# Optimization experiments

Measured on AMD Instinct MI355X. Metric: run time of the kernel, lower is better.

## Reference

```python
import jax, jax.numpy as jnp
import numpy as np

GELU = lambda v: jax.nn.gelu(v, approximate=False)  # torch nn.GELU default (exact erf)


def _gconv(x, w):
    # grouped conv1d, valid padding; w: (C,1,K), groups=C. lax conv = cross-correlation, same as torch.
    return jax.lax.conv_general_dilated(x, w, (1,), [(0, 0)],
                                        dimension_numbers=('NCH', 'OIH', 'NCH'),
                                        feature_group_count=x.shape[1])


def _conv(x, w, b):
    # dense conv1d, kernel 3, padding=1
    y = jax.lax.conv_general_dilated(x, w, (1,), [(1, 1)],
                                     dimension_numbers=('NCH', 'OIH', 'NCH'))
    return y + b[None, :, None]


def setup_inputs() -> dict:
    key = jax.random.key(0)
    ks = jax.random.split(key, 12)
    B, C, L = 8, 64, 2048
    H, FL, HD, TD, level = 32, 8, 64, 16, 3
    Cs = (1 + level) * C  # 256 channels into the ODE
    n = lambda k, s: (jax.random.normal(k, s) * 0.05).astype(jnp.float32)
    z = lambda s: jnp.zeros(s, jnp.float32)
    return dict(
        x=jax.random.normal(ks[0], (B, C, L), jnp.float32),
        # DyWAN_QR params
        sw1=n(ks[1], (H, C)), sb1=z((H,)),
        sw2=n(ks[2], (H, H)), sb2=z((H,)),
        sw3=n(ks[3], (2 * FL, H)), sb3=z((2 * FL,)),
        # ODE time embed / FiLM params
        tw1=n(ks[4], (TD, 1)), tb1=z((TD,)),
        tw2=n(ks[5], (TD, TD)), tb2=z((TD,)),
        cw=n(ks[6], (2 * HD, TD)), cb=z((2 * HD,)),
        # ODE conv stack params
        k1=n(ks[7], (HD, Cs, 3)), kb1=z((HD,)),
        k2=n(ks[8], (HD, HD, 3)), kb2=z((HD,)),
        k3=n(ks[9], (Cs, HD, 3)), kb3=z((Cs,)),
    )


def reference(x, sw1, sb1, sw2, sb2, sw3, sb3, tw1, tb1, tw2, tb2, cw, cb,
              k1, kb1, k2, kb2, k3, kb3):
    B, C, L = x.shape
    level, FL, T = 3, 8, 5

    def dywan(a):
        # stat_net: adaptive max pool over L -> (B,C) -> Linear -> GELU
        feat = GELU(jnp.max(a, axis=-1) @ sw1.T + sb1)
        raw = GELU(feat @ sw2.T + sb2) @ sw3.T + sb3  # (B, 2*FL)
        lo_raw, hi_raw = raw[:, :FL], raw[:, FL:]
        # QR of an (FL,1) column vector == L2 normalization (up to LAPACK sign)
        lo = lo_raw / jnp.linalg.norm(lo_raw, axis=1, keepdims=True)
        hi = hi_raw / jnp.linalg.norm(hi_raw, axis=1, keepdims=True)
        return lo, hi

    pad = FL - 1
    coeffs = [x]
    approx = x
    for _ in range(level):
        lo, hi = dywan(approx)
        lo_f = jnp.broadcast_to(lo.mean(0)[None, None, :], (C, 1, FL))
        hi_f = jnp.broadcast_to(hi.mean(0)[None, None, :], (C, 1, FL))
        ap = jnp.pad(approx, ((0, 0), (0, 0), (pad // 2, pad - pad // 2)), mode='reflect')
        new_approx = _gconv(ap, lo_f)[..., :L]
        coeffs.append(_gconv(ap, hi_f)[..., :L])
        approx = new_approx
    stacked = jnp.concatenate(coeffs, axis=1)  # (B, (1+level)*C, L)

    def ode_f(t, y):
        te = jnp.reshape(t, (1, 1)).astype(y.dtype)
        te = GELU(te @ tw1.T + tb1) @ tw2.T + tb2          # (1, TD)
        cond = te @ cw.T + cb                               # (1, 2*HD)
        hd = cond.shape[1] // 2
        gamma, beta = cond[:, :hd], cond[:, hd:]
        h = _conv(y, k1, kb1)
        h = (1.0 + gamma[:, :, None]) * h + beta[:, :, None]  # FiLM
        h = GELU(h)
        h = GELU(_conv(h, k2, kb2))
        return _conv(h, k3, kb3)

    # dopri5 tableau, fixed grid over linspace(0, 1, T) (b7 = 0, so 6 stages)
    hs = 1.0 / (T - 1)
    y = stacked
    for i in range(T - 1):
        t0 = i * hs
        s1 = ode_f(t0, y)
        s2 = ode_f(t0 + hs / 5, y + hs * (1 / 5) * s1)
        s3 = ode_f(t0 + 3 * hs / 10, y + hs * (3 / 40 * s1 + 9 / 40 * s2))
        s4 = ode_f(t0 + 4 * hs / 5, y + hs * (44 / 45 * s1 - 56 / 15 * s2 + 32 / 9 * s3))
        s5 = ode_f(t0 + 8 * hs / 9, y + hs * (19372 / 6561 * s1 - 25360 / 2187 * s2
                                              + 64448 / 6561 * s3 - 212 / 729 * s4))
        s6 = ode_f(t0 + hs, y + hs * (9017 / 3168 * s1 - 355 / 33 * s2 + 46732 / 5247 * s3
                                      + 49 / 176 * s4 - 5103 / 18656 * s5))
        y = y + hs * (35 / 384 * s1 + 500 / 1113 * s3 + 125 / 192 * s4
                      - 2187 / 6784 * s5 + 11 / 84 * s6)
    ode_out = y

    yl = ode_out[:, :C, :]
    yh0 = ode_out[:, C:2 * C, :]
    yh1 = ode_out[:, 2 * C:3 * C, :]
    yh2 = ode_out[:, 3 * C:4 * C, :]

    dx = ode_f(jnp.float32(1.0), ode_out)
    inner = jnp.sum(stacked * dx, axis=(1, 2))  # (B,)
    ecloss = jnp.mean(inner ** 2)
    return (yl, yh0, yh1, yh2, ecloss)
```

## Files before the change

kernel.cpp:

```cpp
#include <hip/hip_runtime.h>
#include <math.h>

#define B 8
#define C 64
#define L 2048
#define CS 256
#define BCL  (B*C*L)
#define BCSL (B*CS*L)
#define HS 0.25f

typedef unsigned short u16;
typedef unsigned int   u32;
typedef __attribute__((ext_vector_type(8))) short sh8;
typedef __attribute__((ext_vector_type(4))) float f4;
typedef __attribute__((ext_vector_type(8))) unsigned short us8;
typedef __attribute__((ext_vector_type(4))) unsigned short us4;

__device__ __forceinline__ float gelu(float x) {
    return 0.5f * x * (1.0f + erff(x * 0.70710678118654752440f));
}
__device__ __forceinline__ u16 f2b(float f) {
    u32 u = __float_as_uint(f);
    u32 r = u + 0x7FFFu + ((u >> 16) & 1u);
    return (u16)(r >> 16);
}
__device__ __forceinline__ float b2f(u16 h) {
    return __uint_as_float(((u32)h) << 16);
}
__device__ __forceinline__ u32 encmax(float f) {
    u32 b = __float_as_uint(f);
    return (b & 0x80000000u) ? ~b : (b | 0x80000000u);
}
__device__ __forceinline__ float decmax(u32 u) {
    return __uint_as_float((u & 0x80000000u) ? (u ^ 0x80000000u) : ~u);
}

struct ComboB { const u16* p[6]; float c[6]; };

__device__ __forceinline__ void ldw_a6(const sh8* __restrict__ w, int cb, int g,
                                       int lane, sh8 (&A)[6]) {
    #pragma unroll
    for (int u = 0; u < 6; ++u) A[u] = w[((cb + u)*4 + g)*64 + lane];
}

__global__ __launch_bounds__(256) void prep_k(const float* __restrict__ w,
        u16* __restrict__ dst, int IC, int OC) {
    int idx = blockIdx.x * 256 + threadIdx.x;
    int OCG = OC >> 4;
    int j = idx & 7, lane = (idx >> 3) & 63, t = idx >> 9;
    int ocg = t % OCG, c = t / OCG;
    int oc = ocg * 16 + (lane & 15);
    int K = c * 32 + ((lane >> 4) & 3) * 8 + j;
    int kk = K / IC, ic = K % IC;
    dst[idx] = f2b(w[((size_t)oc * IC + ic) * 3 + kk]);
}

__global__ void cond25_k(const float* __restrict__ tw1, const float* __restrict__ tb1,
                         const float* __restrict__ tw2, const float* __restrict__ tb2,
                         const float* __restrict__ cw, const float* __restrict__ cb,
                         float* __restrict__ condall) {
    __shared__ float te1[16], te2[16];
    int tix = blockIdx.x;
    int tid = threadIdx.x;
    double add[6] = {0.0, 0.25/5.0, 3.0*0.25/10.0, 4.0*0.25/5.0, 8.0*0.25/9.0, 0.25};
    float t = (tix == 24) ? 1.0f : (float)((double)(tix / 6) * 0.25 + add[tix % 6]);
    if (tid < 16) te1[tid] = gelu(t * tw1[tid] + tb1[tid]);
    __syncthreads();
    if (tid < 16) {
        float s = tb2[tid];
        for (int k = 0; k < 16; ++k) s += te1[k] * tw2[tid*16+k];
        te2[tid] = s;
    }
    __syncthreads();
    float s = cb[tid];
    for (int j = 0; j < 16; ++j) s += te2[j] * cw[tid*16+j];
    condall[tix*128 + tid] = s;
}

template<int NC, int EPI>
__global__ __launch_bounds__(512, 4) void fused_k(ComboB in,
        const u16* __restrict__ wp1, const float* __restrict__ kb1,
        const u16* __restrict__ wp2, const float* __restrict__ kb2,
        const u16* __restrict__ wp3, const float* __restrict__ kb3,
        const float* __restrict__ condall, int tix,
        u16* __restrict__ outSb,
        float* __restrict__ y, u16* __restrict__ ybout,
        float* __restrict__ outp, const float* __restrict__ stacked,
        double* __restrict__ inner)
{
    __shared__ u16 xs1[50][264];
    __shared__ u16 h1t[50][72];
    __shared__ u16 h2t[34][72];
    __shared__ u16 ypart[32][264];
    __shared__ double sred[8];
    const int tid = threadIdx.x;
    const int l0  = blockIdx.x * 32;
    const int b   = blockIdx.y;
    const int g0  = l0 - 3;

    const float cy1 = HS*(35.f/384.f), cy3 = HS*(500.f/1113.f),
                cy4 = HS*(125.f/192.f), cy5 = -HS*(2187.f/6784.f),
                cy6 = HS*(11.f/84.f);

    const int wave = tid >> 6, lane = tid & 63;
    const int nlo = lane & 15, quad = lane >> 4;
    const int ocg12  = wave & 3;
    const int nfbase = (wave < 4) ? 0 : 2;
    const int nfcnt  = (wave < 4) ? 2 : 1;
    const sh8* w1v = (const sh8*)wp1;
    const sh8* w2v = (const sh8*)wp2;
    const sh8* w3v = (const sh8*)wp3;

    for (int i = tid; i < 12*264; i += 512) xs1[38 + i/264][i%264] = 0;
    if (tid < 144) h1t[48 + tid/72][tid%72] = 0;

    for (int idx = tid; idx < 38*32; idx += 512) {
        int r = idx >> 5, c8 = idx & 31;
        int gl = g0 + r;
        us8 val;
        if (gl >= 0 && gl < L) {
            size_t a = ((size_t)b * L + gl) * 256 + c8 * 8;
            us8 v0 = *(const us8*)(in.p[0] + a);
            if (NC == 1) {
                val = v0;
            } else {
                float f[8];
                float yp[8];
                #pragma unroll
                for (int j = 0; j < 8; ++j) { f[j] = b2f(v0[j]); yp[j] = 0.f; }
                #pragma unroll
                for (int t = 1; t < NC; ++t) {
                    us8 vt = *(const us8*)(in.p[t] + a);
                    #pragma unroll
                    for (int j = 0; j < 8; ++j) {
                        float bv = b2f(vt[j]);
                        f[j] += in.c[t] * bv;
                        if ((EPI == 1 || EPI == 2) && (t == 1 || t == 3 || t == 4 || t == 5)) {
                            float cy = (t == 1) ? cy1 : (t == 3) ? cy3 : (t == 4) ? cy4 : cy5;
                            yp[j] += cy * bv;
                        }
                    }
                }
                #pragma unroll
                for (int j = 0; j < 8; ++j) val[j] = f2b(f[j]);
                if ((EPI == 1 || EPI == 2) && r >= 3 && r < 35) {
                    us8 ypk;
                    #pragma unroll
                    for (int j = 0; j < 8; ++j) ypk[j] = f2b(yp[j]);
                    *(us8*)&ypart[r - 3][c8 * 8] = ypk;
                }
            }
        } else {
            #pragma unroll
            for (int j = 0; j < 8; ++j) val[j] = 0;
        }
        *(us8*)&xs1[r][c8 * 8] = val;
    }

    sh8 A1a[6], A1b[6];
    ldw_a6(w1v, 0, ocg12, lane, A1a);
    __syncthreads();

    f4 a1[2];
    a1[0] = f4{0.f,0.f,0.f,0.f}; a1[1] = a1[0];
    #define C1CHUNK(AA, CB)                                                          \
    {                                                                                \
        _Pragma("unroll")                                                            \
        for (int u_ = 0; u_ < 6; ++u_) {                                             \
            const int c_ = (CB) + u_;                                                \
            const int kk_ = c_ >> 3, ic0_ = (c_ & 7) << 5;                           \
            _Pragma("unroll")                                                        \
            for (int k_ = 0; k_ < 2; ++k_) {                                         \
                if (k_ < nfcnt) {                                                    \
                    const int nf_ = nfbase + k_;                                     \
                    sh8 Bv_ = *(const sh8*)&xs1[nf_*16 + nlo + kk_][ic0_ + quad*8];  \
                    a1[k_] = __builtin_amdgcn_mfma_f32_16x16x32_bf16(AA[u_], Bv_, a1[k_], 0, 0, 0); \
                }                                                                    \
            }                                                                        \
        }                                                                            \
    }
    ldw_a6(w1v, 6, ocg12, lane, A1b);
    C1CHUNK(A1a, 0);
    ldw_a6(w1v, 12, ocg12, lane, A1a);
    C1CHUNK(A1b, 6);
    ldw_a6(w1v, 18, ocg12, lane, A1b);
    C1CHUNK(A1a, 12);
    sh8 A2[6];
    ldw_a6(w2v, 0, ocg12, lane, A2);
    C1CHUNK(A1b, 18);
    #undef C1CHUNK
    {
        const float* cd = condall + tix*128;
        const int oc0 = ocg12*16 + quad*4;
        #pragma unroll
        for (int k = 0; k < 2; ++k) {
            if (k < nfcnt) {
                int nf = nfbase + k;
                int p = nf*16 + nlo;
                int gp = l0 - 2 + p;
                bool ok = (p < 36) && (gp >= 0) && (gp < L);
                us4 pk;
                #pragma unroll
                for (int reg = 0; reg < 4; ++reg) {
                    int oc = oc0 + reg;
                    float v = (1.f + cd[oc]) * (a1[k][reg] + kb1[oc]) + cd[64+oc];
                    pk[reg] = ok ? f2b(gelu(v)) : (u16)0;
                }
                *(us4*)&h1t[p][oc0] = pk;
            }
        }
    }
    __syncthreads();

    f4 a2[2];
    a2[0] = f4{0.f,0.f,0.f,0.f}; a2[1] = a2[0];
    {
        #pragma unroll
        for (int c = 0; c < 6; ++c) {
            int kk = c >> 1, ic0 = (c & 1) << 5;
            #pragma unroll
            for (int k = 0; k < 2; ++k) {
                if (k < nfcnt) {
                    int nf = nfbase + k;
                    sh8 Bv = *(const sh8*)&h1t[nf*16 + nlo + kk][ic0 + quad*8];
                    a2[k] = __builtin_amdgcn_mfma_f32_16x16x32_bf16(A2[c], Bv, a2[k], 0, 0, 0);
                }
            }
        }
    }
    sh8 A3[12];
    #pragma unroll
    for (int i = 0; i < 12; ++i) {
        int c = i >> 1, mf = i & 1;
        A3[i] = w3v[(c*16 + wave*2 + mf)*64 + lane];
    }
    {
        const int oc0 = ocg12*16 + quad*4;
        #pragma unroll
        for (int k = 0; k < 2; ++k) {
            if (k < nfcnt) {
                int nf = nfbase + k;
                int q = nf*16 + nlo;
                if (q < 34) {
                    int gq = l0 - 1 + q;
                    bool ok = (gq >= 0) && (gq < L);
                    us4 pk;
                    #pragma unroll
                    for (int reg = 0; reg < 4; ++reg)
                        pk[reg] = ok ? f2b(gelu(a2[k][reg] + kb2[oc0 + reg])) : (u16)0;
                    *(us4*)&h2t[q][oc0] = pk;
                }
            }
        }
    }
    __syncthreads();

    f4 a3[2][2];
    #pragma unroll
    for (int mf = 0; mf < 2; ++mf) { a3[mf][0] = f4{0.f,0.f,0.f,0.f}; a3[mf][1] = a3[mf][0]; }
    {
        #pragma unroll
        for (int c = 0; c < 6; ++c) {
            int kk = c >> 1, ic0 = (c & 1) << 5;
            sh8 B0 = *(const sh8*)&h2t[nlo + kk][ic0 + quad*8];
            sh8 B1 = *(const sh8*)&h2t[16 + nlo + kk][ic0 + quad*8];
            #pragma unroll
            for (int mf = 0; mf < 2; ++mf) {
                a3[mf][0] = __builtin_amdgcn_mfma_f32_16x16x32_bf16(A3[c*2+mf], B0, a3[mf][0], 0, 0, 0);
                a3[mf][1] = __builtin_amdgcn_mfma_f32_16x16x32_bf16(A3[c*2+mf], B1, a3[mf][1], 0, 0, 0);
            }
        }
    }

    if (EPI == 3) {
        double acc = 0.0;
        #pragma unroll
        for (int mf = 0; mf < 2; ++mf)
            #pragma unroll
            for (int nf = 0; nf < 2; ++nf) {
                int pos = l0 + nf*16 + nlo;
                #pragma unroll
                for (int reg = 0; reg < 4; ++reg) {
                    int oc = (wave*2 + mf)*16 + quad*4 + reg;
                    size_t idx = ((size_t)b*CS + oc)*L + pos;
                    float dx = a3[mf][nf][reg] + kb3[oc];
                    acc += (double)stacked[idx] * (double)dx;
                }
            }
        #pragma unroll
        for (int off = 32; off > 0; off >>= 1) acc += __shfl_down(acc, off, 64);
        if (lane == 0) sred[wave] = acc;
        __syncthreads();
        if (tid == 0) {
            double s = 0.0;
            #pragma unroll
            for (int w = 0; w < 8; ++w) s += sred[w];
            atomicAdd(&inner[b], s);
        }
    } else if (EPI == 0) {
        #pragma unroll
        for (int mf = 0; mf < 2; ++mf) {
            int baseoc = (wave*2 + mf)*16 + quad*4;
            #pragma unroll
            for (int nf = 0; nf < 2; ++nf) {
                int pos = l0 + nf*16 + nlo;
                us4 pk;
                #pragma unroll
                for (int reg = 0; reg < 4; ++reg)
                    pk[reg] = f2b(a3[mf][nf][reg] + kb3[baseoc + reg]);
                *(us4*)(outSb + ((size_t)b*L + pos)*256 + baseoc) = pk;
            }
        }
    } else {
        #pragma unroll
        for (int mf = 0; mf < 2; ++mf) {
            int baseoc = (wave*2 + mf)*16 + quad*4;
            #pragma unroll
            for (int nf = 0; nf < 2; ++nf) {
                int pl = nf*16 + nlo;
                int pos = l0 + pl;
                us4 yp4 = *(const us4*)&ypart[pl][baseoc];
                us4 pk;
                #pragma unroll
                for (int reg = 0; reg < 4; ++reg) {
                    int oc = baseoc + reg;
                    size_t idx = ((size_t)b*CS + oc)*L + pos;
                    float s6 = a3[mf][nf][reg] + kb3[oc];
                    float yv = y[idx] + b2f(yp4[reg]) + cy6 * s6;
                    pk[reg] = f2b(yv);
                    if (EPI == 1) y[idx] = yv;
                    if (EPI == 2) {
                        size_t oidx = (((size_t)(oc >> 6)*B + b)*64 + (oc & 63))*L + pos;
                        outp[oidx] = yv;
                    }
                }
                *(us4*)(ybout + ((size_t)b*L + pos)*256 + baseoc) = pk;
            }
        }
    }
}

__global__ __launch_bounds__(256) void mlp_k(const u32* __restrict__ bm,
    const float* __restrict__ sw1, const float* __restrict__ sb1,
    const float* __restrict__ sw2, const float* __restrict__ sb2,
    const float* __restrict__ sw3, const float* __restrict__ sb3,
    float* __restrict__ filt) {
    __shared__ float m[8][64], f1[8][32], f2[8][32], raw[8][16], nrm[8][2];
    int tid = threadIdx.x;
    for (int i = tid; i < 512; i += 256) m[i >> 6][i & 63] = decmax(bm[i]);
    __syncthreads();
    {
        int b = tid >> 5, h = tid & 31;
        float s = sb1[h];
        for (int c = 0; c < 64; ++c) s += m[b][c] * sw1[h*64+c];
        f1[b][h] = gelu(s);
    }
    __syncthreads();
    {
        int b = tid >> 5, h = tid & 31;
        float s = sb2[h];
        for (int k = 0; k < 32; ++k) s += f1[b][k] * sw2[h*32+k];
        f2[b][h] = gelu(s);
    }
    __syncthreads();
    if (tid < 128) {
        int b = tid >> 4, j = tid & 15;
        float s = sb3[j];
        for (int k = 0; k < 32; ++k) s += f2[b][k] * sw3[j*32+k];
        raw[b][j] = s;
    }
    __syncthreads();
    if (tid < 16) {
        int b = tid >> 1, half = tid & 1;
        float s = 0.f;
        for (int j = 0; j < 8; ++j) { float v = raw[b][half*8+j]; s += v*v; }
        nrm[b][half] = sqrtf(s);
    }
    __syncthreads();
    if (tid < 16) {
        int half = tid >> 3;
        float s = 0.f;
        for (int b = 0; b < 8; ++b) s += raw[b][tid] / nrm[b][half];
        filt[tid] = s * 0.125f;
    }
}

__global__ __launch_bounds__(256) void wconv_k(const float* __restrict__ ap,
    const float* __restrict__ filt, float* __restrict__ apOut,
    float* __restrict__ stacked, int lev, u32* __restrict__ bmaxn) {
    __shared__ float f[16];
    __shared__ float red[256];
    if (threadIdx.x < 16) f[threadIdx.x] = filt[threadIdx.x];
    __syncthreads();
    size_t idx = (size_t)blockIdx.x * 256 + threadIdx.x;
    int l = (int)(idx & 2047);
    size_t bc = idx >> 11;
    int c = (int)(bc & 63), b = (int)(bc >> 6);
    const float* row = ap + (bc << 11);
    float lo = 0.f, hi = 0.f;
    #pragma unroll
    for (int k = 0; k < 8; ++k) {
        int mI = l + k - 3;
        mI = mI < 0 ? -mI : (mI >= L ? 2*L - 2 - mI : mI);
        float v = row[mI];
        lo += v * f[k];
        hi += v * f[8+k];
    }
    stacked[((size_t)b * CS + (size_t)(lev+1) * 64 + c) * L + l] = hi;
    if (bmaxn) {
        apOut[idx] = lo;
        red[threadIdx.x] = lo;
        __syncthreads();
        for (int s = 128; s > 0; s >>= 1) {
            if (threadIdx.x < s) red[threadIdx.x] = fmaxf(red[threadIdx.x], red[threadIdx.x + s]);
            __syncthreads();
        }
        if (threadIdx.x == 0) atomicMax(&bmaxn[blockIdx.x >> 3], encmax(red[0]));
    }
}

__global__ __launch_bounds__(256) void copyx_k(const float* __restrict__ x,
        float* __restrict__ st, u32* __restrict__ bmax0) {
    __shared__ float red[256];
    size_t i = (size_t)blockIdx.x * 256 + threadIdx.x;
    size_t b = i >> 17, rem = i & 131071;
    float v = x[i];
    st[b * ((size_t)CS*L) + rem] = v;
    red[threadIdx.x] = v;
    __syncthreads();
    for (int s = 128; s > 0; s >>= 1) {
        if (threadIdx.x < s) red[threadIdx.x] = fmaxf(red[threadIdx.x], red[threadIdx.x + s]);
        __syncthreads();
    }
    if (threadIdx.x == 0) atomicMax(&bmax0[blockIdx.x >> 3], encmax(red[0]));
}

__global__ __launch_bounds__(256) void tinit_k(const float* __restrict__ st,
        float* __restrict__ y, u16* __restrict__ yb) {
    __shared__ float t[64][65];
    const int tid = threadIdx.x;
    const int l0 = blockIdx.x * 64, c0 = blockIdx.y * 64, b = blockIdx.z;
    #pragma unroll
    for (int k = 0; k < 16; ++k) {
        int c = k * 4 + (tid >> 6), l = tid & 63;
        size_t idx = ((size_t)b*CS + c0 + c) * L + l0 + l;
        float v = st[idx];
        y[idx] = v;
        t[c][l] = v;
    }
    __syncthreads();
    #pragma unroll
    for (int k = 0; k < 16; ++k) {
        int p = k * 4 + (tid >> 6), ch = tid & 63;
        yb[((size_t)b * L + l0 + p) * 256 + c0 + ch] = f2b(t[ch][p]);
    }
}

__global__ void ecfin_k(const double* __restrict__ inner, float* __restrict__ out) {
    double s = 0.0;
    for (int b = 0; b < 8; ++b) s += inner[b] * inner[b];
    out[BCSL] = (float)(s / 8.0);
}

extern "C" void kernel_launch(void* const* d_in, const int* in_sizes, int n_in,
                              void* d_out, int out_size, void* d_ws, size_t ws_size,
                              hipStream_t stream) {
    const float* x   = (const float*)d_in[0];
    const float* sw1 = (const float*)d_in[1];
    const float* sb1 = (const float*)d_in[2];
    const float* sw2 = (const float*)d_in[3];
    const float* sb2 = (const float*)d_in[4];
    const float* sw3 = (const float*)d_in[5];
    const float* sb3 = (const float*)d_in[6];
    const float* tw1 = (const float*)d_in[7];
    const float* tb1 = (const float*)d_in[8];
    const float* tw2 = (const float*)d_in[9];
    const float* tb2 = (const float*)d_in[10];
    const float* cw  = (const float*)d_in[11];
    const float* cb  = (const float*)d_in[12];
    const float* k1  = (const float*)d_in[13];
    const float* kb1 = (const float*)d_in[14];
    const float* k2  = (const float*)d_in[15];
    const float* kb2 = (const float*)d_in[16];
    const float* k3  = (const float*)d_in[17];
    const float* kb3 = (const float*)d_in[18];
    float* out = (float*)d_out;

    char* cur = (char*)d_ws;
    auto alloc = [&](size_t bytes) { void* p = cur; cur += (bytes + 255) & ~(size_t)255; return p; };
    float* stacked = (float*)alloc(BCSL * 4);
    float* y       = (float*)alloc(BCSL * 4);
    u16*   yba     = (u16*)  alloc(BCSL * 2);
    u16*   ybb     = (u16*)  alloc(BCSL * 2);
    u16*   sbuf[5];
    for (int i = 0; i < 5; ++i) sbuf[i] = (u16*)alloc(BCSL * 2);
    float* cond  = (float*)alloc(3200 * 4);
    double* inner = (double*)alloc(8 * 8);
    u32* bmaxe   = (u32*)alloc(3 * 512 * 4);
    float* filt  = (float*)alloc(16 * 4);
    u16* wp1 = (u16*)alloc(49152 * 2);
    u16* wp2 = (u16*)alloc(12288 * 2);
    u16* wp3 = (u16*)alloc(49152 * 2);

    u16 *s1b = sbuf[0], *s2b = sbuf[1], *s3b = sbuf[2], *s4b = sbuf[3], *s5b = sbuf[4];

    hipMemsetAsync(inner, 0, 256 + 3 * 512 * 4, stream);

    prep_k<<<192, 256, 0, stream>>>(k1, wp1, CS, C);
    prep_k<<<48,  256, 0, stream>>>(k2, wp2, C,  C);
    prep_k<<<192, 256, 0, stream>>>(k3, wp3, C,  CS);
    cond25_k<<<25, 128, 0, stream>>>(tw1, tb1, tw2, tb2, cw, cb, cond);

    copyx_k<<<4096, 256, 0, stream>>>(x, stacked, bmaxe);
    const float* apIn = x;
    float* apBuf[2] = {(float*)s1b, (float*)s2b};
    for (int lev = 0; lev < 3; ++lev) {
        mlp_k<<<1, 256, 0, stream>>>(bmaxe + lev*512, sw1, sb1, sw2, sb2, sw3, sb3, filt);
        float* apOut = apBuf[lev & 1];
        wconv_k<<<4096, 256, 0, stream>>>(apIn, filt, apOut, stacked, lev,
                                          (lev < 2) ? (bmaxe + (lev+1)*512) : nullptr);
        apIn = apOut;
    }
    tinit_k<<<dim3(32, 4, 8), 256, 0, stream>>>(stacked, y, yba);

    const float hs = HS;
    dim3 cg(64, 8);
    #define LAUNCH(NC, EPI, CIN, TIX, OUTSB, YBW, OUTP, STK) \
        fused_k<NC, EPI><<<cg, 512, 0, stream>>>(CIN, wp1, kb1, wp2, kb2, wp3, kb3, \
            cond, TIX, OUTSB, y, YBW, OUTP, STK, inner)

    u16* ybs[2] = {yba, ybb};
    for (int i = 0; i < 4; ++i) {
        u16* ybr = ybs[i & 1];
        u16* ybw = ybs[(i & 1) ^ 1];

        ComboB cA{}; cA.p[0] = ybr;
        LAUNCH(1, 0, cA, i*6+0, s1b, nullptr, nullptr, nullptr);

        ComboB cB{}; cB.p[0] = ybr; cB.p[1] = s1b; cB.c[1] = hs*(1.f/5.f);
        LAUNCH(2, 0, cB, i*6+1, s2b, nullptr, nullptr, nullptr);

        ComboB cC{}; cC.p[0] = ybr;
        cC.p[1] = s1b; cC.c[1] = hs*(3.f/40.f);
        cC.p[2] = s2b; cC.c[2] = hs*(9.f/40.f);
        LAUNCH(3, 0, cC, i*6+2, s3b, nullptr, nullptr, nullptr);

        ComboB cD{}; cD.p[0] = ybr;
        cD.p[1] = s1b; cD.c[1] = hs*(44.f/45.f);
        cD.p[2] = s2b; cD.c[2] = -hs*(56.f/15.f);
        cD.p[3] = s3b; cD.c[3] = hs*(32.f/9.f);
        LAUNCH(4, 0, cD, i*6+3, s4b, nullptr, nullptr, nullptr);

        ComboB cE{}; cE.p[0] = ybr;
        cE.p[1] = s1b; cE.c[1] = hs*(19372.f/6561.f);
        cE.p[2] = s2b; cE.c[2] = -hs*(25360.f/2187.f);
        cE.p[3] = s3b; cE.c[3] = hs*(64448.f/6561.f);
        cE.p[4] = s4b; cE.c[4] = -hs*(212.f/729.f);
        LAUNCH(5, 0, cE, i*6+4, s5b, nullptr, nullptr, nullptr);

        ComboB cF{}; cF.p[0] = ybr;
        cF.p[1] = s1b; cF.c[1] = hs*(9017.f/3168.f);
        cF.p[2] = s2b; cF.c[2] = -hs*(355.f/33.f);
        cF.p[3] = s3b; cF.c[3] = hs*(46732.f/5247.f);
        cF.p[4] = s4b; cF.c[4] = hs*(49.f/176.f);
        cF.p[5] = s5b; cF.c[5] = -hs*(5103.f/18656.f);
        if (i < 3) {
            LAUNCH(6, 1, cF, i*6+5, nullptr, ybw, nullptr, nullptr);
        } else {
            LAUNCH(6, 2, cF, i*6+5, nullptr, ybw, out, nullptr);
        }
    }

    ComboB cZ{}; cZ.p[0] = ybs[0];
    LAUNCH(1, 3, cZ, 24, nullptr, nullptr, nullptr, stacked);
    ecfin_k<<<1, 1, 0, stream>>>(inner, out);
    #undef LAUNCH
}
```

Measured before the change: 642.8 us.

## Fuse pairs of RK stages into one kernel using halo recomputation

Each kernel now computes two consecutive Dormand-Prince stages per tile. It widens the input halo from 3 to 6 positions so the first stage's output can be recomputed locally in shared memory and fed straight into the second stage's input combination. This halves the number of stage launches, removes the s5 buffer and its global round trip, and cuts repeated reads of earlier stage buffers. In exchange, the first stage does redundant halo compute on a larger tile (48 positions instead of 32), and more shared memory per block may lower occupancy.

Result: slower. 805.9 us (+25.4%).

```diff
diff --git a/kernel.cpp b/kernel.cpp
--- a/kernel.cpp
+++ b/kernel.cpp
@@ -35,12 +35,130 @@
     return __uint_as_float((u & 0x80000000u) ? (u ^ 0x80000000u) : ~u);
 }
 
-struct ComboB { const u16* p[6]; float c[6]; };
-
 __device__ __forceinline__ void ldw_a6(const sh8* __restrict__ w, int cb, int g,
                                        int lane, sh8 (&A)[6]) {
     #pragma unroll
     for (int u = 0; u < 6; ++u) A[u] = w[((cb + u)*4 + g)*64 + lane];
+}
+
+
+__device__ __forceinline__ void conv1_body(sh8 (&A1a)[6],
+        const sh8* __restrict__ w1v, const sh8* __restrict__ w2v,
+        const float* __restrict__ kb1, const float* __restrict__ cd,
+        const u16 (*__restrict__ IN)[264], u16 (*__restrict__ H1)[72],
+        int n_valid, int gp0, int nfbase, int nfcnt, int ocg12,
+        int nlo, int quad, int lane, sh8 (&A2)[6])
+{
+    f4 a1[2];
+    a1[0] = f4{0.f,0.f,0.f,0.f}; a1[1] = a1[0];
+    sh8 A1b[6];
+    auto chunk = [&](sh8 (&AA)[6], int cb) {
+        #pragma unroll
+        for (int u = 0; u < 6; ++u) {
+            const int c = cb + u;
+            const int kk = c >> 3, ic0 = (c & 7) << 5;
+            #pragma unroll
+            for (int k = 0; k < 2; ++k) {
+                if (k < nfcnt) {
+                    const int nf = nfbase + k;
+                    sh8 Bv = *(const sh8*)&IN[nf*16 + nlo + kk][ic0 + quad*8];
+                    a1[k] = __builtin_amdgcn_mfma_f32_16x16x32_bf16(AA[u], Bv, a1[k], 0, 0, 0);
+                }
+            }
+        }
+    };
+    ldw_a6(w1v, 6, ocg12, lane, A1b);
+    chunk(A1a, 0);
+    ldw_a6(w1v, 12, ocg12, lane, A1a);
+    chunk(A1b, 6);
+    ldw_a6(w1v, 18, ocg12, lane, A1b);
+    chunk(A1a, 12);
+    ldw_a6(w2v, 0, ocg12, lane, A2);
+    chunk(A1b, 18);
+    const int oc0 = ocg12*16 + quad*4;
+    #pragma unroll
+    for (int k = 0; k < 2; ++k) {
+        if (k < nfcnt) {
+            int nf = nfbase + k;
+            int p = nf*16 + nlo;
+            int gp = gp0 + p;
+            bool ok = (p < n_valid) && (gp >= 0) && (gp < L);
+            us4 pk;
+            #pragma unroll
+            for (int reg = 0; reg < 4; ++reg) {
+                int oc = oc0 + reg;
+                float v = (1.f + cd[oc]) * (a1[k][reg] + kb1[oc]) + cd[64+oc];
+                pk[reg] = ok ? f2b(gelu(v)) : (u16)0;
+            }
+            *(us4*)&H1[p][oc0] = pk;
+        }
+    }
+}
+
+__device__ __forceinline__ void conv2_body(sh8 (&A2)[6],
+        const sh8* __restrict__ w3v, const float* __restrict__ kb2,
+        const u16 (*__restrict__ H1)[72], u16 (*__restrict__ H2)[72],
+        int n_valid, int gq0, int nfbase, int nfcnt, int ocg12, int wave,
+        int nlo, int quad, int lane, sh8 (&A3)[12])
+{
+    f4 a2[2];
+    a2[0] = f4{0.f,0.f,0.f,0.f}; a2[1] = a2[0];
+    #pragma unroll
+    for (int c = 0; c < 6; ++c) {
+        int kk = c >> 1, ic0 = (c & 1) << 5;
+        #pragma unroll
+        for (int k = 0; k < 2; ++k) {
+            if (k < nfcnt) {
+                int nf = nfbase + k;
+                sh8 Bv = *(const sh8*)&H1[nf*16 + nlo + kk][ic0 + quad*8];
+                a2[k] = __builtin_amdgcn_mfma_f32_16x16x32_bf16(A2[c], Bv, a2[k], 0, 0, 0);
+            }
+        }
+    }
+    #pragma unroll
+    for (int ii = 0; ii < 12; ++ii) {
+        int c = ii >> 1, mf = ii & 1;
+        A3[ii] = w3v[(c*16 + wave*2 + mf)*64 + lane];
+    }
+    const int oc0 = ocg12*16 + quad*4;
+    #pragma unroll
+    for (int k = 0; k < 2; ++k) {
+        if (k < nfcnt) {
+            int nf = nfbase + k;
+            int q = nf*16 + nlo;
+            int gq = gq0 + q;
+            bool ok = (q < n_valid) && (gq >= 0) && (gq < L);
+            us4 pk;
+            #pragma unroll
+            for (int reg = 0; reg < 4; ++reg)
+                pk[reg] = ok ? f2b(gelu(a2[k][reg] + kb2[oc0 + reg])) : (u16)0;
+            *(us4*)&H2[q][oc0] = pk;
+        }
+    }
+}
+
+template<int NFO>
+__device__ __forceinline__ void conv3_body(sh8 (&A3)[12],
+        const u16 (*__restrict__ H2)[72], f4 (&a3)[2][3], int nlo, int quad)
+{
+    #pragma unroll
+    for (int mf = 0; mf < 2; ++mf)
+        #pragma unroll
+        for (int nf = 0; nf < NFO; ++nf) a3[mf][nf] = f4{0.f,0.f,0.f,0.f};
+    #pragma unroll
+    for (int c = 0; c < 6; ++c) {
+        int kk = c >> 1, ic0 = (c & 1) << 5;
+        sh8 Bf[3];
+        #pragma unroll
+        for (int nf = 0; nf < NFO; ++nf)
+            Bf[nf] = *(const sh8*)&H2[nf*16 + nlo + kk][ic0 + quad*8];
+        #pragma unroll
+        for (int mf = 0; mf < 2; ++mf) {
+            #pragma unroll
+            for (int nf = 0; nf < NFO; ++nf)
+                a3[mf][nf] = __builtin_amdgcn_mfma_f32_16x16x32_bf16(A3[c*2+mf], Bf[nf], a3[mf][nf], 0, 0, 0);
+        }
+    }
 }
 
 __global__ __launch_bounds__(256) void prep_k(const float* __restrict__ w,
@@ -77,31 +195,26 @@
     condall[tix*128 + tid] = s;
 }
 
-template<int NC, int EPI>
-__global__ __launch_bounds__(512, 4) void fused_k(ComboB in,
+template<int P, int EPI>
+__global__ __launch_bounds__(512, 4) void kpair_k(
+        const u16* __restrict__ ybr, u16* __restrict__ ybw,
+        const u16* __restrict__ s1g, const u16* __restrict__ s2g,
+        const u16* __restrict__ s3g, const u16* __restrict__ s4g,
+        u16* __restrict__ sAout, u16* __restrict__ sBout,
         const u16* __restrict__ wp1, const float* __restrict__ kb1,
         const u16* __restrict__ wp2, const float* __restrict__ kb2,
         const u16* __restrict__ wp3, const float* __restrict__ kb3,
-        const float* __restrict__ condall, int tix,
-        u16* __restrict__ outSb,
-        float* __restrict__ y, u16* __restrict__ ybout,
-        float* __restrict__ outp, const float* __restrict__ stacked,
-        double* __restrict__ inner)
+        const float* __restrict__ condall, int tix0,
+        float* __restrict__ y, float* __restrict__ outp)
 {
-    __shared__ u16 xs1[50][264];
-    __shared__ u16 h1t[50][72];
-    __shared__ u16 h2t[34][72];
+    __shared__ u16 CA[50][264];
+    __shared__ u16 SNEW[38][264];
+    __shared__ u16 H1[50][72];
+    __shared__ u16 H2[50][72];
     __shared__ u16 ypart[32][264];
-    __shared__ double sred[8];
     const int tid = threadIdx.x;
     const int l0  = blockIdx.x * 32;
     const int b   = blockIdx.y;
-    const int g0  = l0 - 3;
-
-    const float cy1 = HS*(35.f/384.f), cy3 = HS*(500.f/1113.f),
-                cy4 = HS*(125.f/192.f), cy5 = -HS*(2187.f/6784.f),
-                cy6 = HS*(11.f/84.f);
-
     const int wave = tid >> 6, lane = tid & 63;
     const int nlo = lane & 15, quad = lane >> 4;
     const int ocg12  = wave & 3;
@@ -111,193 +224,156 @@
     const sh8* w2v = (const sh8*)wp2;
     const sh8* w3v = (const sh8*)wp3;
 
-    for (int i = tid; i < 12*264; i += 512) xs1[38 + i/264][i%264] = 0;
-    if (tid < 144) h1t[48 + tid/72][tid%72] = 0;
-
-    for (int idx = tid; idx < 38*32; idx += 512) {
-        int r = idx >> 5, c8 = idx & 31;
-        int gl = g0 + r;
+    const float cy1 = HS*(35.f/384.f), cy3 = HS*(500.f/1113.f),
+                cy4 = HS*(125.f/192.f), cy5 = -HS*(2187.f/6784.f),
+                cy6 = HS*(11.f/84.f);
+    const float cA1 = (P==1) ? HS*(3.f/40.f) : (P==2) ? HS*(19372.f/6561.f) : 0.f;
+    const float cA2 = (P==1) ? HS*(9.f/40.f) : (P==2) ? -HS*(25360.f/2187.f) : 0.f;
+    const float cA3 = (P==2) ? HS*(64448.f/6561.f) : 0.f;
+    const float cA4 = (P==2) ? -HS*(212.f/729.f) : 0.f;
+    const float g1 = (P==1) ? HS*(44.f/45.f)  : (P==2) ? HS*(9017.f/3168.f) : 0.f;
+    const float g2 = (P==1) ? -HS*(56.f/15.f) : (P==2) ? -HS*(355.f/33.f)  : 0.f;
+    const float g3 = (P==2) ? HS*(46732.f/5247.f) : 0.f;
+    const float g4 = (P==2) ? HS*(49.f/176.f) : 0.f;
+    const float gl_ = (P==0) ? HS*(1.f/5.f) : (P==1) ? HS*(32.f/9.f) : -HS*(5103.f/18656.f);
+
+    for (int i2 = tid; i2 < 6*264; i2 += 512) CA[44 + i2/264][i2%264] = 0;
+    if (tid < 144) H1[48 + tid/72][tid%72] = 0;
+    else if (tid < 288) { int t = tid - 144; H2[48 + t/72][t%72] = 0; }
+
+    for (int idx = tid; idx < 44*32; idx += 512) {
+        int r = idx >> 5, o = (idx & 31) * 8;
+        int gl = l0 - 6 + r;
         us8 val;
         if (gl >= 0 && gl < L) {
-            size_t a = ((size_t)b * L + gl) * 256 + c8 * 8;
-            us8 v0 = *(const us8*)(in.p[0] + a);
-            if (NC == 1) {
+            size_t a = ((size_t)b * L + gl) * 256 + o;
+            us8 v0 = *(const us8*)(ybr + a);
+            if (P == 0) {
                 val = v0;
             } else {
                 float f[8];
-                float yp[8];
-                #pragma unroll
-                for (int j = 0; j < 8; ++j) { f[j] = b2f(v0[j]); yp[j] = 0.f; }
-                #pragma unroll
-                for (int t = 1; t < NC; ++t) {
-                    us8 vt = *(const us8*)(in.p[t] + a);
+                #pragma unroll
+                for (int j = 0; j < 8; ++j) f[j] = b2f(v0[j]);
+                us8 v1 = *(const us8*)(s1g + a);
+                #pragma unroll
+                for (int j = 0; j < 8; ++j) f[j] += cA1 * b2f(v1[j]);
+                us8 v2 = *(const us8*)(s2g + a);
+                #pragma unroll
+                for (int j = 0; j < 8; ++j) f[j] += cA2 * b2f(v2[j]);
+                if (P == 2) {
+                    us8 v3 = *(const us8*)(s3g + a);
                     #pragma unroll
-                    for (int j = 0; j < 8; ++j) {
-                        float bv = b2f(vt[j]);
-                        f[j] += in.c[t] * bv;
-                        if ((EPI == 1 || EPI == 2) && (t == 1 || t == 3 || t == 4 || t == 5)) {
-                            float cy = (t == 1) ? cy1 : (t == 3) ? cy3 : (t == 4) ? cy4 : cy5;
-                            yp[j] += cy * bv;
-                        }
-                    }
+                    for (int j = 0; j < 8; ++j) f[j] += cA3 * b2f(v3[j]);
+                    us8 v4 = *(const us8*)(s4g + a);
+                    #pragma unroll
+                    for (int j = 0; j < 8; ++j) f[j] += cA4 * b2f(v4[j]);
                 }
                 #pragma unroll
                 for (int j = 0; j < 8; ++j) val[j] = f2b(f[j]);
-                if ((EPI == 1 || EPI == 2) && r >= 3 && r < 35) {
-                    us8 ypk;
-                    #pragma unroll
-                    for (int j = 0; j < 8; ++j) ypk[j] = f2b(yp[j]);
-                    *(us8*)&ypart[r - 3][c8 * 8] = ypk;
+            }
+        } else {
+            #pragma unroll
+            for (int j = 0; j < 8; ++j) val[j] = 0;
+        }
+        *(us8*)&CA[r][o] = val;
+    }
+
+    sh8 A1a[6], A2[6], A3[12];
+    ldw_a6(w1v, 0, ocg12, lane, A1a);
+    __syncthreads();
+
+    conv1_body(A1a, w1v, w2v, kb1, condall + tix0*128, CA, H1,
+               42, l0-5, nfbase, nfcnt, ocg12, nlo, quad, lane, A2);
+    __syncthreads();
+    conv2_body(A2, w3v, kb2, H1, H2, 40, l0-4, nfbase, nfcnt, ocg12, wave,
+               nlo, quad, lane, A3);
+    __syncthreads();
+    {
+        f4 a3[2][3];
+        conv3_body<3>(A3, H2, a3, nlo, quad);
+        #pragma unroll
+        for (int mf = 0; mf < 2; ++mf) {
+            const int oc0 = (wave*2 + mf)*16 + quad*4;
+            #pragma unroll
+            for (int nf = 0; nf < 3; ++nf) {
+                const int m = nf*16 + nlo;
+                const int gm = l0 - 3 + m;
+                const bool ok = (gm >= 0) && (gm < L);
+                us4 pk;
+                #pragma unroll
+                for (int reg = 0; reg < 4; ++reg)
+                    pk[reg] = ok ? f2b(a3[mf][nf][reg] + kb3[oc0 + reg]) : (u16)0;
+                if (m < 38) *(us4*)&SNEW[m][oc0] = pk;
+                if (P < 2 && m >= 3 && m < 35)
+                    *(us4*)(sAout + ((size_t)b*L + gm)*256 + oc0) = pk;
+            }
+        }
+    }
+    __syncthreads();
+
+    for (int idx = tid; idx < 38*32; idx += 512) {
+        int r = idx >> 5, o = (idx & 31) * 8;
+        int gl = l0 - 3 + r;
+        us8 sv = *(const us8*)&SNEW[r][o];
+        us8 val;
+        if (gl >= 0 && gl < L) {
+            size_t a = ((size_t)b * L + gl) * 256 + o;
+            us8 v0 = *(const us8*)(ybr + a);
+            float f[8];
+            #pragma unroll
+            for (int j = 0; j < 8; ++j) f[j] = b2f(v0[j]);
+            us8 v1, v3, v4;
+            if (P >= 1) {
+                v1 = *(const us8*)(s1g + a);
+                #pragma unroll
+                for (int j = 0; j < 8; ++j) f[j] += g1 * b2f(v1[j]);
+                us8 v2 = *(const us8*)(s2g + a);
+                #pragma unroll
+                for (int j = 0; j < 8; ++j) f[j] += g2 * b2f(v2[j]);
+            }
+            if (P == 2) {
+                v3 = *(const us8*)(s3g + a);
+                #pragma unroll
+                for (int j = 0; j < 8; ++j) f[j] += g3 * b2f(v3[j]);
+                v4 = *(const us8*)(s4g + a);
+                #pragma unroll
+                for (int j = 0; j < 8; ++j) f[j] += g4 * b2f(v4[j]);
+            }
+            #pragma unroll
+            for (int j = 0; j < 8; ++j) f[j] += gl_ * b2f(sv[j]);
+            #pragma unroll
+            for (int j = 0; j < 8; ++j) val[j] = f2b(f[j]);
+            if (P == 2 && r >= 3 && r < 35) {
+                us8 ypk;
+                #pragma unroll
+                for (int j = 0; j < 8; ++j) {
+                    float yp = cy1 * b2f(v1[j]);
+                    yp += cy3 * b2f(v3[j]);
+                    yp += cy4 * b2f(v4[j]);
+                    yp += cy5 * b2f(sv[j]);
+                    ypk[j] = f2b(yp);
                 }
+                *(us8*)&ypart[r - 3][o] = ypk;
             }
         } else {
             #pragma unroll
             for (int j = 0; j < 8; ++j) val[j] = 0;
         }
-        *(us8*)&xs1[r][c8 * 8] = val;
-    }
-
-    sh8 A1a[6], A1b[6];
+        *(us8*)&CA[r][o] = val;
+    }
     ldw_a6(w1v, 0, ocg12, lane, A1a);
     __syncthreads();
 
-    f4 a1[2];
-    a1[0] = f4{0.f,0.f,0.f,0.f}; a1[1] = a1[0];
-    #define C1CHUNK(AA, CB)                                                          \
-    {                                                                                \
-        _Pragma("unroll")                                                            \
-        for (int u_ = 0; u_ < 6; ++u_) {                                             \
-            const int c_ = (CB) + u_;                                                \
-            const int kk_ = c_ >> 3, ic0_ = (c_ & 7) << 5;                           \
-            _Pragma("unroll")                                                        \
-            for (int k_ = 0; k_ < 2; ++k_) {                                         \
-                if (k_ < nfcnt) {                                                    \
-                    const int nf_ = nfbase + k_;                                     \
-                    sh8 Bv_ = *(const sh8*)&xs1[nf_*16 + nlo + kk_][ic0_ + quad*8];  \
-                    a1[k_] = __builtin_amdgcn_mfma_f32_16x16x32_bf16(AA[u_], Bv_, a1[k_], 0, 0, 0); \
-                }                                                                    \
-            }                                                                        \
-        }                                                                            \
-    }
-    ldw_a6(w1v, 6, ocg12, lane, A1b);
-    C1CHUNK(A1a, 0);
-    ldw_a6(w1v, 12, ocg12, lane, A1a);
-    C1CHUNK(A1b, 6);
-    ldw_a6(w1v, 18, ocg12, lane, A1b);
-    C1CHUNK(A1a, 12);
-    sh8 A2[6];
-    ldw_a6(w2v, 0, ocg12, lane, A2);
-    C1CHUNK(A1b, 18);
-    #undef C1CHUNK
-    {
-        const float* cd = condall + tix*128;
-        const int oc0 = ocg12*16 + quad*4;
-        #pragma unroll
-        for (int k = 0; k < 2; ++k) {
-            if (k < nfcnt) {
-                int nf = nfbase + k;
-                int p = nf*16 + nlo;
-                int gp = l0 - 2 + p;
-                bool ok = (p < 36) && (gp >= 0) && (gp < L);
-                us4 pk;
-                #pragma unroll
-                for (int reg = 0; reg < 4; ++reg) {
-                    int oc = oc0 + reg;
-                    float v = (1.f + cd[oc]) * (a1[k][reg] + kb1[oc]) + cd[64+oc];
-                    pk[reg] = ok ? f2b(gelu(v)) : (u16)0;
-                }
-                *(us4*)&h1t[p][oc0] = pk;
-            }
-        }
-    }
-    __syncthreads();
-
-    f4 a2[2];
-    a2[0] = f4{0.f,0.f,0.f,0.f}; a2[1] = a2[0];
-    {
-        #pragma unroll
-        for (int c = 0; c < 6; ++c) {
-            int kk = c >> 1, ic0 = (c & 1) << 5;
-            #pragma unroll
-            for (int k = 0; k < 2; ++k) {
-                if (k < nfcnt) {
-                    int nf = nfbase + k;
-                    sh8 Bv = *(const sh8*)&h1t[nf*16 + nlo + kk][ic0 + quad*8];
-                    a2[k] = __builtin_amdgcn_mfma_f32_16x16x32_bf16(A2[c], Bv, a2[k], 0, 0, 0);
-                }
-            }
-        }
-    }
-    sh8 A3[12];
-    #pragma unroll
-    for (int i = 0; i < 12; ++i) {
-        int c = i >> 1, mf = i & 1;
-        A3[i] = w3v[(c*16 + wave*2 + mf)*64 + lane];
-    }
-    {
-        const int oc0 = ocg12*16 + quad*4;
-        #pragma unroll
-        for (int k = 0; k < 2; ++k) {
-            if (k < nfcnt) {
-                int nf = nfbase + k;
-                int q = nf*16 + nlo;
-                if (q < 34) {
-                    int gq = l0 - 1 + q;
-                    bool ok = (gq >= 0) && (gq < L);
-                    us4 pk;
-                    #pragma unroll
-                    for (int reg = 0; reg < 4; ++reg)
-                        pk[reg] = ok ? f2b(gelu(a2[k][reg] + kb2[oc0 + reg])) : (u16)0;
-                    *(us4*)&h2t[q][oc0] = pk;
-                }
-            }
-        }
-    }
-    __syncthreads();
-
-    f4 a3[2][2];
-    #pragma unroll
-    for (int mf = 0; mf < 2; ++mf) { a3[mf][0] = f4{0.f,0.f,0.f,0.f}; a3[mf][1] = a3[mf][0]; }
-    {
-        #pragma unroll
-        for (int c = 0; c < 6; ++c) {
-            int kk = c >> 1, ic0 = (c & 1) << 5;
-            sh8 B0 = *(const sh8*)&h2t[nlo + kk][ic0 + quad*8];
-            sh8 B1 = *(const sh8*)&h2t[16 + nlo + kk][ic0 + quad*8];
-            #pragma unroll
-            for (int mf = 0; mf < 2; ++mf) {
-                a3[mf][0] = __builtin_amdgcn_mfma_f32_16x16x32_bf16(A3[c*2+mf], B0, a3[mf][0], 0, 0, 0);
-                a3[mf][1] = __builtin_amdgcn_mfma_f32_16x16x32_bf16(A3[c*2+mf], B1, a3[mf][1], 0, 0, 0);
-            }
-        }
-    }
-
-    if (EPI == 3) {
-        double acc = 0.0;
-        #pragma unroll
-        for (int mf = 0; mf < 2; ++mf)
-            #pragma unroll
-            for (int nf = 0; nf < 2; ++nf) {
-                int pos = l0 + nf*16 + nlo;
-                #pragma unroll
-                for (int reg = 0; reg < 4; ++reg) {
-                    int oc = (wave*2 + mf)*16 + quad*4 + reg;
-                    size_t idx = ((size_t)b*CS + oc)*L + pos;
-                    float dx = a3[mf][nf][reg] + kb3[oc];
-                    acc += (double)stacked[idx] * (double)dx;
-                }
-            }
-        #pragma unroll
-        for (int off = 32; off > 0; off >>= 1) acc += __shfl_down(acc, off, 64);
-        if (lane == 0) sred[wave] = acc;
-        __syncthreads();
-        if (tid == 0) {
-            double s = 0.0;
-            #pragma unroll
-            for (int w = 0; w < 8; ++w) s += sred[w];
-            atomicAdd(&inner[b], s);
-        }
-    } else if (EPI == 0) {
+    conv1_body(A1a, w1v, w2v, kb1, condall + (tix0+1)*128, CA, H1,
+               36, l0-2, nfbase, nfcnt, ocg12, nlo, quad, lane, A2);
+    __syncthreads();
+    conv2_body(A2, w3v, kb2, H1, H2, 34, l0-1, nfbase, nfcnt, ocg12, wave,
+               nlo, quad, lane, A3);
+    __syncthreads();
+    f4 a3[2][3];
+    conv3_body<2>(A3, H2, a3, nlo, quad);
+
+    if (EPI == 0) {
         #pragma unroll
         for (int mf = 0; mf < 2; ++mf) {
             int baseoc = (wave*2 + mf)*16 + quad*4;
@@ -308,7 +384,7 @@
                 #pragma unroll
                 for (int reg = 0; reg < 4; ++reg)
                     pk[reg] = f2b(a3[mf][nf][reg] + kb3[baseoc + reg]);
-                *(us4*)(outSb + ((size_t)b*L + pos)*256 + baseoc) = pk;
+                *(us4*)(sBout + ((size_t)b*L + pos)*256 + baseoc) = pk;
             }
         }
     } else {
@@ -334,9 +410,86 @@
                         outp[oidx] = yv;
                     }
                 }
-                *(us4*)(ybout + ((size_t)b*L + pos)*256 + baseoc) = pk;
-            }
-        }
+                *(us4*)(ybw + ((size_t)b*L + pos)*256 + baseoc) = pk;
+            }
+        }
+    }
+}
+
+__global__ __launch_bounds__(512, 4) void ec_k(const u16* __restrict__ ybin,
+        const u16* __restrict__ wp1, const float* __restrict__ kb1,
+        const u16* __restrict__ wp2, const float* __restrict__ kb2,
+        const u16* __restrict__ wp3, const float* __restrict__ kb3,
+        const float* __restrict__ condall,
+        const float* __restrict__ stacked, double* __restrict__ inner)
+{
+    __shared__ u16 CA[50][264];
+    __shared__ u16 H1[50][72];
+    __shared__ u16 H2[50][72];
+    __shared__ double sred[8];
+    const int tid = threadIdx.x;
+    const int l0  = blockIdx.x * 32;
+    const int b   = blockIdx.y;
+    const int wave = tid >> 6, lane = tid & 63;
+    const int nlo = lane & 15, quad = lane >> 4;
+    const int ocg12  = wave & 3;
+    const int nfbase = (wave < 4) ? 0 : 2;
+    const int nfcnt  = (wave < 4) ? 2 : 1;
+    const sh8* w1v = (const sh8*)wp1;
+    const sh8* w2v = (const sh8*)wp2;
+    const sh8* w3v = (const sh8*)wp3;
+
+    for (int i2 = tid; i2 < 12*264; i2 += 512) CA[38 + i2/264][i2%264] = 0;
+    if (tid < 144) H1[48 + tid/72][tid%72] = 0;
+    else if (tid < 288) { int t = tid - 144; H2[48 + t/72][t%72] = 0; }
+
+    for (int idx = tid; idx < 38*32; idx += 512) {
+        int r = idx >> 5, o = (idx & 31) * 8;
+        int gl = l0 - 3 + r;
+        us8 v;
+        if (gl >= 0 && gl < L) {
+            v = *(const us8*)(ybin + ((size_t)b*L + gl)*256 + o);
+        } else {
+            #pragma unroll
+            for (int j = 0; j < 8; ++j) v[j] = 0;
+        }
+        *(us8*)&CA[r][o] = v;
+    }
+    sh8 A1a[6], A2[6], A3[12];
+    ldw_a6(w1v, 0, ocg12, lane, A1a);
+    __syncthreads();
+    conv1_body(A1a, w1v, w2v, kb1, condall + 24*128, CA, H1,
+               36, l0-2, nfbase, nfcnt, ocg12, nlo, quad, lane, A2);
+    __syncthreads();
+    conv2_body(A2, w3v, kb2, H1, H2, 34, l0-1, nfbase, nfcnt, ocg12, wave,
+               nlo, quad, lane, A3);
+    __syncthreads();
+    f4 a3[2][3];
+    conv3_body<2>(A3, H2, a3, nlo, quad);
+
+    double acc = 0.0;
+    #pragma unroll
+    for (int mf = 0; mf < 2; ++mf)
+        #pragma unroll
+        for (int nf = 0; nf < 2; ++nf) {
+            int pos = l0 + nf*16 + nlo;
+            #pragma unroll
+            for (int reg = 0; reg < 4; ++reg) {
+                int oc = (wave*2 + mf)*16 + quad*4 + reg;
+                size_t idx = ((size_t)b*CS + oc)*L + pos;
+                float dx = a3[mf][nf][reg] + kb3[oc];
+                acc += (double)stacked[idx] * (double)dx;
+            }
+        }
+    #pragma unroll
+    for (int off = 32; off > 0; off >>= 1) acc += __shfl_down(acc, off, 64);
+    if (lane == 0) sred[wave] = acc;
+    __syncthreads();
+    if (tid == 0) {
+        double s = 0.0;
+        #pragma unroll
+        for (int w = 0; w < 8; ++w) s += sred[w];
+        atomicAdd(&inner[b], s);
     }
 }
 
@@ -492,8 +645,10 @@
     float* y       = (float*)alloc(BCSL * 4);
     u16*   yba     = (u16*)  alloc(BCSL * 2);
     u16*   ybb     = (u16*)  alloc(BCSL * 2);
-    u16*   sbuf[5];
-    for (int i = 0; i < 5; ++i) sbuf[i] = (u16*)alloc(BCSL * 2);
+    u16*   s1b     = (u16*)  alloc(BCSL * 2);
+    u16*   s2b     = (u16*)  alloc(BCSL * 2);
+    u16*   s3b     = (u16*)  alloc(BCSL * 2);
+    u16*   s4b     = (u16*)  alloc(BCSL * 2);
     float* cond  = (float*)alloc(3200 * 4);
     double* inner = (double*)alloc(8 * 8);
     u32* bmaxe   = (u32*)alloc(3 * 512 * 4);
@@ -501,8 +656,6 @@
     u16* wp1 = (u16*)alloc(49152 * 2);
     u16* wp2 = (u16*)alloc(12288 * 2);
     u16* wp3 = (u16*)alloc(49152 * 2);
-
-    u16 *s1b = sbuf[0], *s2b = sbuf[1], *s3b = sbuf[2], *s4b = sbuf[3], *s5b = sbuf[4];
 
     hipMemsetAsync(inner, 0, 256 + 3 * 512 * 4, stream);
 
@@ -523,56 +676,25 @@
     }
     tinit_k<<<dim3(32, 4, 8), 256, 0, stream>>>(stacked, y, yba);
 
-    const float hs = HS;
     dim3 cg(64, 8);
-    #define LAUNCH(NC, EPI, CIN, TIX, OUTSB, YBW, OUTP, STK) \
-        fused_k<NC, EPI><<<cg, 512, 0, stream>>>(CIN, wp1, kb1, wp2, kb2, wp3, kb3, \
-            cond, TIX, OUTSB, y, YBW, OUTP, STK, inner)
-
     u16* ybs[2] = {yba, ybb};
     for (int i = 0; i < 4; ++i) {
         u16* ybr = ybs[i & 1];
         u16* ybw = ybs[(i & 1) ^ 1];
 
-        ComboB cA{}; cA.p[0] = ybr;
-        LAUNCH(1, 0, cA, i*6+0, s1b, nullptr, nullptr, nullptr);
-
-        ComboB cB{}; cB.p[0] = ybr; cB.p[1] = s1b; cB.c[1] = hs*(1.f/5.f);
-        LAUNCH(2, 0, cB, i*6+1, s2b, nullptr, nullptr, nullptr);
-
-        ComboB cC{}; cC.p[0] = ybr;
-        cC.p[1] = s1b; cC.c[1] = hs*(3.f/40.f);
-        cC.p[2] = s2b; cC.c[2] = hs*(9.f/40.f);
-        LAUNCH(3, 0, cC, i*6+2, s3b, nullptr, nullptr, nullptr);
-
-        ComboB cD{}; cD.p[0] = ybr;
-        cD.p[1] = s1b; cD.c[1] = hs*(44.f/45.f);
-        cD.p[2] = s2b; cD.c[2] = -hs*(56.f/15.f);
-        cD.p[3] = s3b; cD.c[3] = hs*(32.f/9.f);
-        LAUNCH(4, 0, cD, i*6+3, s4b, nullptr, nullptr, nullptr);
-
-        ComboB cE{}; cE.p[0] = ybr;
-        cE.p[1] = s1b; cE.c[1] = hs*(19372.f/6561.f);
-        cE.p[2] = s2b; cE.c[2] = -hs*(25360.f/2187.f);
-        cE.p[3] = s3b; cE.c[3] = hs*(64448.f/6561.f);
-        cE.p[4] = s4b; cE.c[4] = -hs*(212.f/729.f);
-        LAUNCH(5, 0, cE, i*6+4, s5b, nullptr, nullptr, nullptr);
-
-        ComboB cF{}; cF.p[0] = ybr;
-        cF.p[1] = s1b; cF.c[1] = hs*(9017.f/3168.f);
-        cF.p[2] = s2b; cF.c[2] = -hs*(355.f/33.f);
-        cF.p[3] = s3b; cF.c[3] = hs*(46732.f/5247.f);
-        cF.p[4] = s4b; cF.c[4] = hs*(49.f/176.f);
-        cF.p[5] = s5b; cF.c[5] = -hs*(5103.f/18656.f);
-        if (i < 3) {
-            LAUNCH(6, 1, cF, i*6+5, nullptr, ybw, nullptr, nullptr);
-        } else {
-            LAUNCH(6, 2, cF, i*6+5, nullptr, ybw, out, nullptr);
-        }
-    }
-
-    ComboB cZ{}; cZ.p[0] = ybs[0];
-    LAUNCH(1, 3, cZ, 24, nullptr, nullptr, nullptr, stacked);
+        kpair_k<0, 0><<<cg, 512, 0, stream>>>(ybr, nullptr, s1b, s2b, s3b, s4b,
+                s1b, s2b, wp1, kb1, wp2, kb2, wp3, kb3, cond, i*6+0, nullptr, nullptr);
+        kpair_k<1, 0><<<cg, 512, 0, stream>>>(ybr, nullptr, s1b, s2b, s3b, s4b,
+                s3b, s4b, wp1, kb1, wp2, kb2, wp3, kb3, cond, i*6+2, nullptr, nullptr);
+        if (i < 3)
+            kpair_k<2, 1><<<cg, 512, 0, stream>>>(ybr, ybw, s1b, s2b, s3b, s4b,
+                    nullptr, nullptr, wp1, kb1, wp2, kb2, wp3, kb3, cond, i*6+4, y, nullptr);
+        else
+            kpair_k<2, 2><<<cg, 512, 0, stream>>>(ybr, ybw, s1b, s2b, s3b, s4b,
+                    nullptr, nullptr, wp1, kb1, wp2, kb2, wp3, kb3, cond, i*6+4, y, out);
+    }
+
+    ec_k<<<cg, 512, 0, stream>>>(ybs[0], wp1, kb1, wp2, kb2, wp3, kb3,
+                                 cond, stacked, inner);
     ecfin_k<<<1, 1, 0, stream>>>(inner, out);
-    #undef LAUNCH
-}
+}
```
